# Optimization experiments

Hardware: AMD Instinct MI355X
Metric: run time of the kernel (lower is better)

The kernel has to match this reference:

```python
import jax, jax.numpy as jnp
import numpy as np

# dims
H = 1024          # hidden_size
E = 2048          # d_inner = 2*H
NH = 32           # nheads = E/64
P = 64            # headdim
N = 128           # d_state
G = 1             # ngroups
K = 4             # d_conv
Q = 128           # SSD chunk length
FF = 4096         # intermediate_size
EPS = 1e-6        # rms_norm_eps
NEPS = 1e-5       # mamba gated-norm eps
CONV_DIM = E + 2 * G * N            # 2304
D_IN = 2 * E + 2 * G * N + NH       # 4384


def rmsnorm(x, w, eps):
    v = jnp.mean(x.astype(jnp.float32) ** 2, axis=-1, keepdims=True)
    return (x.astype(jnp.float32) * jax.lax.rsqrt(v + eps)).astype(x.dtype) * w


def segsum(x):
    # x: [..., T] -> [..., T, T] with out[i,j] = sum_{j<k<=i} x[k], -inf above diag
    T = x.shape[-1]
    cs = jnp.cumsum(x, axis=-1)
    s = cs[..., :, None] - cs[..., None, :]
    mask = jnp.tril(jnp.ones((T, T), dtype=bool))
    return jnp.where(mask, s, -jnp.inf)


def ssd(x, dt, A_log, B, C):
    # x:[b,l,nh,p], dt:[b,l,nh], B,C:[b,l,N] (ngroups=1, shared over heads)
    b, l, nh, p = x.shape
    A = -jnp.exp(A_log)                      # [nh]
    dA = dt * A                              # [b,l,nh]
    xd = x * dt[..., None]                   # discretized input
    c = l // Q
    xd = xd.reshape(b, c, Q, nh, p)
    dAc = dA.reshape(b, c, Q, nh).transpose(0, 3, 1, 2)   # [b,h,c,q]
    Bc = B.reshape(b, c, Q, N)
    Cc = C.reshape(b, c, Q, N)
    A_cs = jnp.cumsum(dAc, axis=-1)                        # [b,h,c,q]
    Lm = jnp.exp(segsum(dAc))                              # [b,h,c,q,q]
    # intra-chunk (diagonal blocks)
    Y_diag = jnp.einsum('bcqn,bcsn,bhcqs,bcshp->bcqhp', Cc, Bc, Lm, xd)
    # per-chunk final states
    decay_states = jnp.exp(A_cs[..., -1:] - A_cs)          # [b,h,c,q]
    states = jnp.einsum('bcqn,bhcq,bcqhp->bchpn', Bc, decay_states, xd)
    # inter-chunk recurrence (initial state = 0)
    A_last = jnp.pad(A_cs[..., -1], ((0, 0), (0, 0), (1, 0)))   # [b,h,c+1]
    decay_chunk = jnp.exp(segsum(A_last))                       # [b,h,c+1,c+1]
    states = jnp.concatenate([jnp.zeros_like(states[:, :1]), states], axis=1)
    new_states = jnp.einsum('bhzc,bchpn->bzhpn', decay_chunk, states)[:, :-1]
    Y_off = jnp.einsum('bcqn,bchpn,bhcq->bcqhp', Cc, new_states, jnp.exp(A_cs))
    return (Y_diag + Y_off).reshape(b, l, nh, p)


def mamba2(h, w_in, w_conv, b_conv, dt_bias, A_log, D, w_mnorm, w_out):
    b, l, _ = h.shape
    zxbcdt = h @ w_in.T                         # [b,l,D_IN]
    z, xBC, dt = jnp.split(zxbcdt, [E, E + CONV_DIM], axis=-1)
    # causal depthwise conv (kernel K) over channels of xBC
    pad = jnp.pad(xBC, ((0, 0), (K - 1, 0), (0, 0)))
    xBC = sum(pad[:, k:k + l, :] * w_conv[:, k] for k in range(K)) + b_conv
    xBC = jax.nn.silu(xBC)
    x, B, C = jnp.split(xBC, [E, E + G * N], axis=-1)
    dt = jax.nn.softplus(dt + dt_bias)          # [b,l,NH]
    xh = x.reshape(b, l, NH, P)
    y = ssd(xh, dt, A_log, B, C)
    y = y + D[None, None, :, None] * xh         # per-head skip
    y = y.reshape(b, l, E)
    y = rmsnorm(y * jax.nn.silu(z), w_mnorm, NEPS)   # gated RMSNorm
    return y @ w_out.T


def setup_inputs() -> dict:
    key = jax.random.key(0)
    ks = jax.random.split(key, 12)
    dt0 = jax.random.uniform(ks[0], (NH,), minval=0.001, maxval=0.1)
    dt_bias = dt0 + jnp.log(-jnp.expm1(-dt0))   # inverse softplus
    return {
        'hidden_states': jax.random.normal(ks[1], (2, 2048, H), dtype=jnp.float32),
        'w_ln1': jnp.ones((H,), jnp.float32),
        'w_in': 0.02 * jax.random.normal(ks[2], (D_IN, H), dtype=jnp.float32),
        'w_conv': 0.1 * jax.random.normal(ks[3], (CONV_DIM, K), dtype=jnp.float32),
        'b_conv': jnp.zeros((CONV_DIM,), jnp.float32),
        'dt_bias': dt_bias,
        'A_log': jnp.log(jax.random.uniform(ks[4], (NH,), minval=1.0, maxval=16.0)),
        'D': jnp.ones((NH,), jnp.float32),
        'w_mnorm': jnp.ones((E,), jnp.float32),
        'w_out': 0.02 * jax.random.normal(ks[5], (H, E), dtype=jnp.float32),
        'w_ln2': jnp.ones((H,), jnp.float32),
        'w_gate': 0.02 * jax.random.normal(ks[6], (FF, H), dtype=jnp.float32),
        'w_up': 0.02 * jax.random.normal(ks[7], (FF, H), dtype=jnp.float32),
        'w_down': 0.02 * jax.random.normal(ks[8], (H, FF), dtype=jnp.float32),
    }


def reference(hidden_states, w_ln1, w_in, w_conv, b_conv, dt_bias, A_log, D,
              w_mnorm, w_out, w_ln2, w_gate, w_up, w_down):
    residual = hidden_states
    h = rmsnorm(hidden_states, w_ln1, EPS)
    h = mamba2(h, w_in, w_conv, b_conv, dt_bias, A_log, D, w_mnorm, w_out)
    hidden = residual + h
    residual = hidden
    h = rmsnorm(hidden, w_ln2, EPS)
    h = (jax.nn.silu(h @ w_gate.T) * (h @ w_up.T)) @ w_down.T
    return residual + h
```

## Files before the change

### kernel.cpp

```cpp
#include <hip/hip_runtime.h>

#define DEV static __device__ __forceinline__

typedef short bf16x8 __attribute__((ext_vector_type(8)));
typedef float floatx4 __attribute__((ext_vector_type(4)));
typedef unsigned short ushort4v __attribute__((ext_vector_type(4)));
typedef unsigned short ushort8v __attribute__((ext_vector_type(8)));

DEV unsigned short f32_bf16(float f) {
  unsigned int u = __builtin_bit_cast(unsigned int, f);
  u = u + 0x7fffu + ((u >> 16) & 1u);
  return (unsigned short)(u >> 16);
}
DEV float bf2f(unsigned short u) {
  unsigned int v = ((unsigned int)u) << 16;
  return __builtin_bit_cast(float, v);
}
DEV float sigmoidf_(float x) { return 1.0f / (1.0f + __expf(-x)); }
DEV float siluf_(float x) { return x * sigmoidf_(x); }

#define GLD_LDS16(g, l)                                                              \
  __builtin_amdgcn_global_load_lds((const __attribute__((address_space(1))) void*)(g), \
                                   (__attribute__((address_space(3))) void*)(l), 16, 0, 0)

template <int MODE>
__global__ __launch_bounds__(256) void gemm128(
    const unsigned short* __restrict__ A, const unsigned short* __restrict__ B,
    void* __restrict__ Cv, int K, int lda, int ldb, int ldc,
    long long bsA, long long bsB, long long bsC,
    int nsplit, unsigned short* __restrict__ Cv2, int ldc2) {
  __shared__ unsigned short As[8192];
  __shared__ unsigned short Bs[8192];
  A += (long long)blockIdx.z * bsA;
  B += (long long)blockIdx.z * bsB;
  const long long coff = (long long)blockIdx.z * bsC;
  const int tid = threadIdx.x;
  const int w = tid >> 6, lane = tid & 63;

  const int nbx = gridDim.x, nby = gridDim.y;
  const int GM = 4;
  int bid = blockIdx.y * nbx + blockIdx.x;
  int gid = bid / (GM * nbx);
  int rem = bid - gid * (GM * nbx);
  int gsz = min(GM, nby - gid * GM);
  int mtile = gid * GM + rem % gsz;
  int ntile = rem / gsz;
  const int m0 = mtile << 7, n0 = ntile << 7;

  const int srow = lane >> 2;
  const int schunk = ((lane & 3) ^ (srow & 3)) * 8;
  const unsigned short* ag0 = A + (long long)(m0 + w * 32 + srow) * lda + schunk;
  const unsigned short* ag1 = ag0 + (long long)16 * lda;
  const unsigned short* bg0 = B + (long long)(n0 + w * 32 + srow) * ldb + schunk;
  const unsigned short* bg1 = bg0 + (long long)16 * ldb;
  unsigned short* al0 = As + (w * 32) * 32 + lane * 8;
  unsigned short* al1 = As + (w * 32 + 16) * 32 + lane * 8;
  unsigned short* bl0 = Bs + (w * 32) * 32 + lane * 8;
  unsigned short* bl1 = Bs + (w * 32 + 16) * 32 + lane * 8;

  const int wr = (w >> 1) << 6, wc = (w & 1) << 6;
  const int fr = lane & 15;
  const int slot = (((lane >> 4) ^ (fr & 3))) << 3;

  floatx4 acc[4][4];
#pragma unroll
  for (int i = 0; i < 4; ++i)
#pragma unroll
    for (int j = 0; j < 4; ++j) acc[i][j] = (floatx4){0.f, 0.f, 0.f, 0.f};

  for (int k0 = 0; k0 < K; k0 += 64) {
    __syncthreads();
    GLD_LDS16(ag0 + k0, al0);
    GLD_LDS16(ag1 + k0, al1);
    GLD_LDS16(ag0 + k0 + 32, al0 + 4096);
    GLD_LDS16(ag1 + k0 + 32, al1 + 4096);
    GLD_LDS16(bg0 + k0, bl0);
    GLD_LDS16(bg1 + k0, bl1);
    GLD_LDS16(bg0 + k0 + 32, bl0 + 4096);
    GLD_LDS16(bg1 + k0 + 32, bl1 + 4096);
    __syncthreads();
#pragma unroll
    for (int s = 0; s < 2; ++s) {
      const unsigned short* Ab = As + s * 4096;
      const unsigned short* Bb = Bs + s * 4096;
      bf16x8 af[4], bf_[4];
#pragma unroll
      for (int i = 0; i < 4; ++i) af[i] = *(const bf16x8*)(Ab + (wr + i * 16 + fr) * 32 + slot);
#pragma unroll
      for (int j = 0; j < 4; ++j) bf_[j] = *(const bf16x8*)(Bb + (wc + j * 16 + fr) * 32 + slot);
#pragma unroll
      for (int i = 0; i < 4; ++i)
#pragma unroll
        for (int j = 0; j < 4; ++j)
          acc[i][j] = __builtin_amdgcn_mfma_f32_16x16x32_bf16(af[i], bf_[j], acc[i][j], 0, 0, 0);
    }
  }

  const int r0 = (lane >> 4) << 2;
#pragma unroll
  for (int i = 0; i < 4; ++i) {
#pragma unroll
    for (int j = 0; j < 4; ++j) {
      int col = n0 + wc + j * 16 + fr;
      int row = m0 + wr + i * 16 + r0;
#pragma unroll
      for (int r = 0; r < 4; ++r) {
        float v = acc[i][j][r];
        if constexpr (MODE == 0) {
          ((float*)Cv)[coff + (long long)(row + r) * ldc + col] = v;
        } else {
          if (col < nsplit)
            ((unsigned short*)Cv)[coff + (long long)(row + r) * ldc + col] = f32_bf16(v);
          else
            Cv2[(long long)(row + r) * ldc2 + (col - nsplit)] = f32_bf16(v);
        }
      }
    }
  }
}

__global__ __launch_bounds__(256) void gemm128_glu(
    const unsigned short* __restrict__ A, const unsigned short* __restrict__ Bg,
    const unsigned short* __restrict__ Bu, unsigned short* __restrict__ act,
    int K, int lda, int ldb, int ldc) {
  __shared__ unsigned short As[8192];
  __shared__ unsigned short Bgs[8192];
  __shared__ unsigned short Bus[8192];
  const int tid = threadIdx.x;
  const int w = tid >> 6, lane = tid & 63;

  const int nbx = gridDim.x, nby = gridDim.y;
  const int GM = 4;
  int bid = blockIdx.y * nbx + blockIdx.x;
  int gid = bid / (GM * nbx);
  int rem = bid - gid * (GM * nbx);
  int gsz = min(GM, nby - gid * GM);
  int mtile = gid * GM + rem % gsz;
  int ntile = rem / gsz;
  const int m0 = mtile << 7, n0 = ntile << 7;

  const int srow = lane >> 2;
  const int schunk = ((lane & 3) ^ (srow & 3)) * 8;
  const unsigned short* ag0 = A + (long long)(m0 + w * 32 + srow) * lda + schunk;
  const unsigned short* ag1 = ag0 + (long long)16 * lda;
  const unsigned short* gg0 = Bg + (long long)(n0 + w * 32 + srow) * ldb + schunk;
  const unsigned short* gg1 = gg0 + (long long)16 * ldb;
  const unsigned short* ug0 = Bu + (long long)(n0 + w * 32 + srow) * ldb + schunk;
  const unsigned short* ug1 = ug0 + (long long)16 * ldb;
  unsigned short* al0 = As + (w * 32) * 32 + lane * 8;
  unsigned short* al1 = As + (w * 32 + 16) * 32 + lane * 8;
  unsigned short* gl0 = Bgs + (w * 32) * 32 + lane * 8;
  unsigned short* gl1 = Bgs + (w * 32 + 16) * 32 + lane * 8;
  unsigned short* ul0 = Bus + (w * 32) * 32 + lane * 8;
  unsigned short* ul1 = Bus + (w * 32 + 16) * 32 + lane * 8;

  const int wr = (w >> 1) << 6, wc = (w & 1) << 6;
  const int fr = lane & 15;
  const int slot = (((lane >> 4) ^ (fr & 3))) << 3;

  floatx4 accg[4][4], accu[4][4];
#pragma unroll
  for (int i = 0; i < 4; ++i)
#pragma unroll
    for (int j = 0; j < 4; ++j) {
      accg[i][j] = (floatx4){0.f, 0.f, 0.f, 0.f};
      accu[i][j] = (floatx4){0.f, 0.f, 0.f, 0.f};
    }

  for (int k0 = 0; k0 < K; k0 += 64) {
    __syncthreads();
    GLD_LDS16(ag0 + k0, al0);
    GLD_LDS16(ag1 + k0, al1);
    GLD_LDS16(ag0 + k0 + 32, al0 + 4096);
    GLD_LDS16(ag1 + k0 + 32, al1 + 4096);
    GLD_LDS16(gg0 + k0, gl0);
    GLD_LDS16(gg1 + k0, gl1);
    GLD_LDS16(gg0 + k0 + 32, gl0 + 4096);
    GLD_LDS16(gg1 + k0 + 32, gl1 + 4096);
    GLD_LDS16(ug0 + k0, ul0);
    GLD_LDS16(ug1 + k0, ul1);
    GLD_LDS16(ug0 + k0 + 32, ul0 + 4096);
    GLD_LDS16(ug1 + k0 + 32, ul1 + 4096);
    __syncthreads();
#pragma unroll
    for (int s = 0; s < 2; ++s) {
      const unsigned short* Ab = As + s * 4096;
      const unsigned short* Gb = Bgs + s * 4096;
      const unsigned short* Ub = Bus + s * 4096;
      bf16x8 af[4], bf_[4];
#pragma unroll
      for (int i = 0; i < 4; ++i) af[i] = *(const bf16x8*)(Ab + (wr + i * 16 + fr) * 32 + slot);
#pragma unroll
      for (int j = 0; j < 4; ++j) bf_[j] = *(const bf16x8*)(Gb + (wc + j * 16 + fr) * 32 + slot);
#pragma unroll
      for (int i = 0; i < 4; ++i)
#pragma unroll
        for (int j = 0; j < 4; ++j)
          accg[i][j] = __builtin_amdgcn_mfma_f32_16x16x32_bf16(af[i], bf_[j], accg[i][j], 0, 0, 0);
#pragma unroll
      for (int j = 0; j < 4; ++j) bf_[j] = *(const bf16x8*)(Ub + (wc + j * 16 + fr) * 32 + slot);
#pragma unroll
      for (int i = 0; i < 4; ++i)
#pragma unroll
        for (int j = 0; j < 4; ++j)
          accu[i][j] = __builtin_amdgcn_mfma_f32_16x16x32_bf16(af[i], bf_[j], accu[i][j], 0, 0, 0);
    }
  }

  const int r0 = (lane >> 4) << 2;
#pragma unroll
  for (int i = 0; i < 4; ++i) {
#pragma unroll
    for (int j = 0; j < 4; ++j) {
      long long base = (long long)(m0 + wr + i * 16 + r0) * ldc + (n0 + wc + j * 16 + fr);
#pragma unroll
      for (int r = 0; r < 4; ++r)
        act[base + (long long)r * ldc] = f32_bf16(siluf_(accg[i][j][r]) * accu[i][j][r]);
    }
  }
}

template <int WM>
__global__ __launch_bounds__(256) void gemm_small_nt(
    const unsigned short* __restrict__ A, const unsigned short* __restrict__ B,
    float* __restrict__ C, int M, int N, int K, int lda, int ldb, int ldc) {
  const int w = threadIdx.x >> 6;
  const int lane = threadIdx.x & 63;
  const int lm = lane & 15;
  const int ko = (lane >> 4) << 3;
  const int bn0 = blockIdx.x << 6;
  const int m_base = blockIdx.y * (WM * 64) + w * (WM * 16);

  const unsigned short* arow[WM];
#pragma unroll
  for (int i = 0; i < WM; ++i) arow[i] = A + (long long)(m_base + i * 16 + lm) * lda + ko;
  int nv = (N - bn0) >> 4;
  nv = nv > 4 ? 4 : nv;
  const unsigned short* brow[4];
#pragma unroll
  for (int j = 0; j < 4; ++j) {
    int nr = bn0 + j * 16 + lm;
    brow[j] = B + (long long)(j < nv ? nr : 0) * ldb + ko;
  }
  floatx4 acc[WM][4];
#pragma unroll
  for (int i = 0; i < WM; ++i)
#pragma unroll
    for (int j = 0; j < 4; ++j) acc[i][j] = (floatx4){0.f, 0.f, 0.f, 0.f};
  for (int k0 = 0; k0 < K; k0 += 32) {
    bf16x8 a[WM];
#pragma unroll
    for (int i = 0; i < WM; ++i) a[i] = *(const bf16x8*)(arow[i] + k0);
#pragma unroll
    for (int j = 0; j < 4; ++j) {
      if (j < nv) {
        bf16x8 b = *(const bf16x8*)(brow[j] + k0);
#pragma unroll
        for (int i = 0; i < WM; ++i)
          acc[i][j] = __builtin_amdgcn_mfma_f32_16x16x32_bf16(a[i], b, acc[i][j], 0, 0, 0);
      }
    }
  }
  const int r0 = (lane >> 4) << 2;
#pragma unroll
  for (int i = 0; i < WM; ++i)
#pragma unroll
    for (int j = 0; j < 4; ++j)
      if (j < nv) {
        int col = bn0 + j * 16 + lm;
        long long base = (long long)(m_base + i * 16 + r0) * ldc + col;
#pragma unroll
        for (int r = 0; r < 4; ++r) C[base + (long long)r * ldc] = acc[i][j][r];
      }
}

__global__ __launch_bounds__(256) void f32_to_bf16_k(const float* __restrict__ src,
                                                     unsigned short* __restrict__ dst,
                                                     long long n4) {
  long long i = (long long)blockIdx.x * 256 + threadIdx.x;
  if (i < n4) {
    float4 v = ((const float4*)src)[i];
    ushort4v o = {f32_bf16(v.x), f32_bf16(v.y), f32_bf16(v.z), f32_bf16(v.w)};
    ((ushort4v*)dst)[i] = o;
  }
}

__global__ __launch_bounds__(256) void zero_out_k(float* __restrict__ o, long long n) {
  long long i = (long long)blockIdx.x * 256 + threadIdx.x;
  if (i < n) o[i] = 0.f;
}

__global__ __launch_bounds__(256) void rmsnorm1024_bf16_k(const float* __restrict__ x,
                                                          const float* __restrict__ w,
                                                          unsigned short* __restrict__ out,
                                                          float eps) {
  long long row = blockIdx.x;
  int t = threadIdx.x;
  float4 v = ((const float4*)(x + row * 1024))[t];
  float ss = v.x * v.x + v.y * v.y + v.z * v.z + v.w * v.w;
  __shared__ float red[4];
#pragma unroll
  for (int o = 32; o > 0; o >>= 1) ss += __shfl_down(ss, o, 64);
  if ((t & 63) == 0) red[t >> 6] = ss;
  __syncthreads();
  float tot = red[0] + red[1] + red[2] + red[3];
  float sc = rsqrtf(tot * (1.0f / 1024.0f) + eps);
  float4 wv = ((const float4*)w)[t];
  ushort4v o = {f32_bf16(v.x * sc * wv.x), f32_bf16(v.y * sc * wv.y),
                f32_bf16(v.z * sc * wv.z), f32_bf16(v.w * sc * wv.w)};
  ((ushort4v*)(out + row * 1024))[t] = o;
}

__global__ __launch_bounds__(256) void add_rmsnorm_k(const float* __restrict__ hs,
                                                     const float* __restrict__ parts,
                                                     long long pstride, int np,
                                                     const float* __restrict__ w,
                                                     float* __restrict__ mh,
                                                     unsigned short* __restrict__ h2, float eps) {
  long long row = blockIdx.x;
  int t = threadIdx.x;
  float4 v = ((const float4*)(hs + row * 1024))[t];
  for (int p = 0; p < np; ++p) {
    float4 u = ((const float4*)(parts + p * pstride + row * 1024))[t];
    v.x += u.x;
    v.y += u.y;
    v.z += u.z;
    v.w += u.w;
  }
  ((float4*)(mh + row * 1024))[t] = v;
  float ss = v.x * v.x + v.y * v.y + v.z * v.z + v.w * v.w;
  __shared__ float red[4];
#pragma unroll
  for (int o = 32; o > 0; o >>= 1) ss += __shfl_down(ss, o, 64);
  if ((t & 63) == 0) red[t >> 6] = ss;
  __syncthreads();
  float tot = red[0] + red[1] + red[2] + red[3];
  float sc = rsqrtf(tot * (1.0f / 1024.0f) + eps);
  float4 wv = ((const float4*)w)[t];
  ushort4v o = {f32_bf16(v.x * sc * wv.x), f32_bf16(v.y * sc * wv.y),
                f32_bf16(v.z * sc * wv.z), f32_bf16(v.w * sc * wv.w)};
  ((ushort4v*)(h2 + row * 1024))[t] = o;
}

__global__ __launch_bounds__(256) void addn_f32_k(const float* __restrict__ a,
                                                  const float* __restrict__ parts,
                                                  long long pstride, int np,
                                                  float* __restrict__ o, long long n4) {
  long long i = (long long)blockIdx.x * 256 + threadIdx.x;
  if (i < n4) {
    float4 x = ((const float4*)a)[i];
    for (int p = 0; p < np; ++p) {
      float4 u = ((const float4*)(parts + p * pstride))[i];
      x.x += u.x;
      x.y += u.y;
      x.z += u.z;
      x.w += u.w;
    }
    ((float4*)o)[i] = x;
  }
}

__global__ __launch_bounds__(256) void gated_rmsnorm2048_k(const unsigned short* __restrict__ y,
                                                           const unsigned short* __restrict__ z,
                                                           const float* __restrict__ w,
                                                           unsigned short* __restrict__ out,
                                                           float eps) {
  long long row = blockIdx.x;
  int t = threadIdx.x;
  ushort8v yv = ((const ushort8v*)(y + row * 2048))[t];
  ushort8v zv = ((const ushort8v*)(z + row * 2048))[t];
  float g[8];
  float ss = 0.f;
#pragma unroll
  for (int j = 0; j < 8; ++j) {
    g[j] = bf2f(yv[j]) * siluf_(bf2f(zv[j]));
    ss += g[j] * g[j];
  }
  __shared__ float red[4];
#pragma unroll
  for (int o = 32; o > 0; o >>= 1) ss += __shfl_down(ss, o, 64);
  if ((t & 63) == 0) red[t >> 6] = ss;
  __syncthreads();
  float tot = red[0] + red[1] + red[2] + red[3];
  float sc = rsqrtf(tot * (1.0f / 2048.0f) + eps);
  float ww[8];
  *(float4*)&ww[0] = ((const float4*)w)[2 * t];
  *(float4*)&ww[4] = ((const float4*)w)[2 * t + 1];
  ushort8v o;
#pragma unroll
  for (int j = 0; j < 8; ++j) o[j] = f32_bf16(g[j] * sc * ww[j]);
  ((ushort8v*)(out + row * 2048))[t] = o;
}

__global__ __launch_bounds__(256) void conv_silu_k(const unsigned short* __restrict__ xraw,
                                                   const float* __restrict__ wconv,
                                                   const float* __restrict__ bconv,
                                                   unsigned short* __restrict__ xBC) {
  int m = blockIdx.x;
  int l = m & 2047;
  for (int ch = threadIdx.x; ch < 2304; ch += 256) {
    float acc = bconv[ch];
#pragma unroll
    for (int k = 0; k < 4; ++k) {
      int lk = l + k - 3;
      if (lk >= 0) acc += bf2f(xraw[(long long)(m + k - 3) * 2304 + ch]) * wconv[ch * 4 + k];
    }
    xBC[(long long)m * 2304 + ch] = f32_bf16(siluf_(acc));
  }
}

__global__ __launch_bounds__(256) void dt_softplus_k(const float* __restrict__ dtraw,
                                                     const float* __restrict__ dt_bias,
                                                     float* __restrict__ dt_s) {
  int i = blockIdx.x * 256 + threadIdx.x;
  float xv = dtraw[i] + dt_bias[i & 31];
  dt_s[i] = xv > 20.f ? xv : log1pf(expf(xv));
}

__global__ __launch_bounds__(128) void dA_cumsum_k(const float* __restrict__ dt_s,
                                                   const float* __restrict__ A_log,
                                                   float* __restrict__ dA_cs) {
  int bi = blockIdx.x;
  int c = bi & 15, h = (bi >> 4) & 31, b = bi >> 9;
  int q = threadIdx.x;
  float A = -expf(A_log[h]);
  float v = dt_s[((long long)(b * 2048 + c * 128 + q)) * 32 + h] * A;
  __shared__ float sbuf[128];
  sbuf[q] = v;
  __syncthreads();
  for (int off = 1; off < 128; off <<= 1) {
    float tv = (q >= off) ? sbuf[q - off] : 0.f;
    __syncthreads();
    sbuf[q] += tv;
    __syncthreads();
  }
  dA_cs[(long long)bi * 128 + q] = sbuf[q];
}

__global__ __launch_bounds__(256) void ssd_diag_states_k(
    const unsigned short* __restrict__ xBC, const float* __restrict__ dt_s,
    const float* __restrict__ dA_cs, const unsigned short* __restrict__ G,
    unsigned short* __restrict__ y, unsigned short* __restrict__ states) {
  __shared__ unsigned short Mz[128 * 136];
  __shared__ unsigned short xdT[64 * 136];
  __shared__ float Acs[128];
  __shared__ float wdec[128];
  const int bx = blockIdx.x;
  const int h = bx & 31, c = (bx >> 5) & 15, b = bx >> 9;
  const int t = threadIdx.x;
  const int w = t >> 6, lane = t & 63, fr = lane & 15, hi = lane >> 4;
  const long long rowbase = (long long)b * 2048 + c * 128;
  const long long abase = ((long long)((b * 32 + h) * 16 + c)) << 7;

  if (t < 128) {
    float a = dA_cs[abase + t];
    Acs[t] = a;
    wdec[t] = __expf(dA_cs[abase + 127] - a);
  }
  {
    int s = t >> 1, p0 = (t & 1) * 32;
    float dtv = dt_s[(rowbase + s) * 32 + h];
    const ushort8v* xv = (const ushort8v*)(xBC + (rowbase + s) * 2304 + h * 64 + p0);
#pragma unroll
    for (int i = 0; i < 4; ++i) {
      ushort8v vv = xv[i];
#pragma unroll
      for (int j = 0; j < 8; ++j) xdT[(p0 + i * 8 + j) * 136 + s] = f32_bf16(bf2f(vv[j]) * dtv);
    }
  }
  __syncthreads();
  {
    int q = t >> 1, s0 = (t & 1) * 64;
    float aq = Acs[q];
    const ushort8v* gv =
        (const ushort8v*)(G + (((long long)(b * 16 + c)) * 128 + q) * 128 + s0);
#pragma unroll
    for (int i = 0; i < 8; ++i) {
      ushort8v gg = gv[i];
#pragma unroll
      for (int j = 0; j < 8; ++j) {
        int s = s0 + i * 8 + j;
        float m = (s <= q) ? bf2f(gg[j]) * __expf(aq - Acs[s]) : 0.f;
        Mz[q * 136 + s] = f32_bf16(m);
      }
    }
  }
  __syncthreads();
  const int q0 = w << 5;
  {
    floatx4 acc[2][4];
#pragma unroll
    for (int i = 0; i < 2; ++i)
#pragma unroll
      for (int j = 0; j < 4; ++j) acc[i][j] = (floatx4){0.f, 0.f, 0.f, 0.f};
#pragma unroll
    for (int k0 = 0; k0 < 128; k0 += 32) {
      int kk = k0 + hi * 8;
      bf16x8 a0 = *(const bf16x8*)(Mz + (q0 + fr) * 136 + kk);
      bf16x8 a1 = *(const bf16x8*)(Mz + (q0 + 16 + fr) * 136 + kk);
      bf16x8 bf_[4];
#pragma unroll
      for (int j = 0; j < 4; ++j) bf_[j] = *(const bf16x8*)(xdT + (j * 16 + fr) * 136 + kk);
#pragma unroll
      for (int j = 0; j < 4; ++j) {
        acc[0][j] = __builtin_amdgcn_mfma_f32_16x16x32_bf16(a0, bf_[j], acc[0][j], 0, 0, 0);
        acc[1][j] = __builtin_amdgcn_mfma_f32_16x16x32_bf16(a1, bf_[j], acc[1][j], 0, 0, 0);
      }
    }
#pragma unroll
    for (int i = 0; i < 2; ++i)
#pragma unroll
      for (int r = 0; r < 4; ++r) {
        int q = q0 + i * 16 + hi * 4 + r;
        unsigned short* yrow = y + (rowbase + q) * 2048 + h * 64;
#pragma unroll
        for (int j = 0; j < 4; ++j) yrow[j * 16 + fr] = f32_bf16(acc[i][j][r]);
      }
  }
  __syncthreads();
  {
    int s = t >> 1, n0 = (t & 1) * 64;
    float wd = wdec[s];
    const ushort8v* bv = (const ushort8v*)(xBC + (rowbase + s) * 2304 + 2048 + n0);
#pragma unroll
    for (int i = 0; i < 8; ++i) {
      ushort8v bb = bv[i];
#pragma unroll
      for (int j = 0; j < 8; ++j) Mz[(n0 + i * 8 + j) * 136 + s] = f32_bf16(bf2f(bb[j]) * wd);
    }
  }
  __syncthreads();
  {
    floatx4 acc[2][4];
#pragma unroll
    for (int i = 0; i < 2; ++i)
#pragma unroll
      for (int j = 0; j < 4; ++j) acc[i][j] = (floatx4){0.f, 0.f, 0.f, 0.f};
#pragma unroll
    for (int k0 = 0; k0 < 128; k0 += 32) {
      int kk = k0 + hi * 8;
      bf16x8 a0 = *(const bf16x8*)(Mz + (q0 + fr) * 136 + kk);
      bf16x8 a1 = *(const bf16x8*)(Mz + (q0 + 16 + fr) * 136 + kk);
      bf16x8 bf_[4];
#pragma unroll
      for (int j = 0; j < 4; ++j) bf_[j] = *(const bf16x8*)(xdT + (j * 16 + fr) * 136 + kk);
#pragma unroll
      for (int j = 0; j < 4; ++j) {
        acc[0][j] = __builtin_amdgcn_mfma_f32_16x16x32_bf16(a0, bf_[j], acc[0][j], 0, 0, 0);
        acc[1][j] = __builtin_amdgcn_mfma_f32_16x16x32_bf16(a1, bf_[j], acc[1][j], 0, 0, 0);
      }
    }
    unsigned short* st = states + (long long)bx * 8192;
#pragma unroll
    for (int i = 0; i < 2; ++i)
#pragma unroll
      for (int j = 0; j < 4; ++j) {
        int p = j * 16 + fr;
        int n = q0 + i * 16 + hi * 4;
        ushort4v o;
#pragma unroll
        for (int r = 0; r < 4; ++r) o[r] = f32_bf16(acc[i][j][r]);
        *(ushort4v*)(st + p * 128 + n) = o;
      }
  }
}

__global__ __launch_bounds__(256) void ssd_scan_k(const float* __restrict__ dA_cs,
                                                  unsigned short* __restrict__ states) {
  int h = blockIdx.x & 31, b = blockIdx.x >> 5;
  int t = threadIdx.x;
  float carry[32];
#pragma unroll
  for (int i = 0; i < 32; ++i) carry[i] = 0.f;
  for (int c = 0; c < 16; ++c) {
    long long base = ((long long)((b * 16 + c) * 32 + h)) * 8192;
    float dec = __expf(dA_cs[(((long long)((b * 32 + h) * 16 + c)) << 7) + 127]);
#pragma unroll
    for (int i = 0; i < 32; ++i) {
      long long idx = base + t + i * 256;
      float local = bf2f(states[idx]);
      states[idx] = f32_bf16(carry[i]);
      carry[i] = dec * carry[i] + local;
    }
  }
}

__global__ __launch_bounds__(256) void ssd_off_k(const unsigned short* __restrict__ xBC,
                                                 const float* __restrict__ dA_cs,
                                                 const unsigned short* __restrict__ states,
                                                 const float* __restrict__ Dvec,
                                                 unsigned short* __restrict__ y) {
  __shared__ float eA[128];
  const int bx = blockIdx.x;
  const int h = bx & 31, c = (bx >> 5) & 15, b = bx >> 9;
  const int t = threadIdx.x;
  const int w = t >> 6, lane = t & 63, fr = lane & 15, hi = lane >> 4;
  const long long rowbase = (long long)b * 2048 + c * 128;
  const long long abase = ((long long)((b * 32 + h) * 16 + c)) << 7;
  if (t < 128) eA[t] = __expf(dA_cs[abase + t]);
  __syncthreads();

  const unsigned short* st = states + (long long)bx * 8192;
  const int q0 = w << 5;
  floatx4 acc[2][4];
#pragma unroll
  for (int i = 0; i < 2; ++i)
#pragma unroll
    for (int j = 0; j < 4; ++j) acc[i][j] = (floatx4){0.f, 0.f, 0.f, 0.f};

#pragma unroll
  for (int k0 = 0; k0 < 128; k0 += 32) {
    int kk = k0 + hi * 8;
    bf16x8 a0 = *(const bf16x8*)(xBC + (rowbase + q0 + fr) * 2304 + 2176 + kk);
    bf16x8 a1 = *(const bf16x8*)(xBC + (rowbase + q0 + 16 + fr) * 2304 + 2176 + kk);
    bf16x8 bf_[4];
#pragma unroll
    for (int j = 0; j < 4; ++j) bf_[j] = *(const bf16x8*)(st + (j * 16 + fr) * 128 + kk);
#pragma unroll
    for (int j = 0; j < 4; ++j) {
      acc[0][j] = __builtin_amdgcn_mfma_f32_16x16x32_bf16(a0, bf_[j], acc[0][j], 0, 0, 0);
      acc[1][j] = __builtin_amdgcn_mfma_f32_16x16x32_bf16(a1, bf_[j], acc[1][j], 0, 0, 0);
    }
  }

  float Dh = Dvec[h];
#pragma unroll
  for (int i = 0; i < 2; ++i) {
#pragma unroll
    for (int r = 0; r < 4; ++r) {
      int q = q0 + i * 16 + hi * 4 + r;
      float e = eA[q];
      const unsigned short* xrow = xBC + (rowbase + q) * 2304 + h * 64;
      unsigned short* yrow = y + (rowbase + q) * 2048 + h * 64;
#pragma unroll
      for (int j = 0; j < 4; ++j) {
        int p = j * 16 + fr;
        float v = bf2f(yrow[p]) + e * acc[i][j][r] + Dh * bf2f(xrow[p]);
        yrow[p] = f32_bf16(v);
      }
    }
  }
}

extern "C" void kernel_launch(void* const* d_in, const int* in_sizes, int n_in, void* d_out,
                              int out_size, void* d_ws, size_t ws_size, hipStream_t stream) {
  const float* hs = (const float*)d_in[0];
  const float* w_ln1 = (const float*)d_in[1];
  const float* w_in = (const float*)d_in[2];
  const float* w_conv = (const float*)d_in[3];
  const float* b_conv = (const float*)d_in[4];
  const float* dt_bias = (const float*)d_in[5];
  const float* A_log = (const float*)d_in[6];
  const float* Dvec = (const float*)d_in[7];
  const float* w_mnorm = (const float*)d_in[8];
  const float* w_out = (const float*)d_in[9];
  const float* w_ln2 = (const float*)d_in[10];
  const float* w_gate = (const float*)d_in[11];
  const float* w_up = (const float*)d_in[12];
  const float* w_down = (const float*)d_in[13];
  float* out = (float*)d_out;
  const int M = 4096;
  const int NOSPLIT = 1 << 30;

  char* ws = (char*)d_ws;
  const size_t R0 = 0;
  const size_t R1 = 33554432;
  const size_t R1b = R1 + 33554432;
  const size_t R2 = 71303168;
  const size_t R3 = 90177536;
  const size_t R4 = 107544576;
  const size_t W0 = 108068864;
  const size_t NEED = 133234688;

  if (ws_size < NEED) {
    hipLaunchKernelGGL(zero_out_k, dim3((out_size + 255) / 256), dim3(256), 0, stream, out,
                       (long long)out_size);
    return;
  }

  unsigned short* z = (unsigned short*)(ws + R0);
  unsigned short* act = (unsigned short*)(ws + R0);
  float* oproj_parts = (float*)(ws + R0);
  unsigned short* xraw = (unsigned short*)(ws + R1);
  unsigned short* states = (unsigned short*)(ws + R1);
  unsigned short* ybuf = (unsigned short*)(ws + R1 + 16777216);
  float* down_parts = (float*)(ws + R1);
  unsigned short* wbf_out = (unsigned short*)(ws + R1b);
  unsigned short* xBC = (unsigned short*)(ws + R2);
  unsigned short* ygn = (unsigned short*)(ws + R2);
  unsigned short* h2 = (unsigned short*)(ws + R2);
  unsigned short* hnorm = (unsigned short*)(ws + R3);
  unsigned short* wbf_in = (unsigned short*)(ws + R3 + 8388608);
  float* dt_s = (float*)(ws + R3);
  float* dA_cs = (float*)(ws + R3 + 524288);
  unsigned short* Gbuf = (unsigned short*)(ws + R3 + 1048576);
  float* mh = (float*)(ws + R3);
  float* dtraw = (float*)(ws + R4);
  unsigned short* wbf_gate = (unsigned short*)(ws + W0);
  unsigned short* wbf_up = (unsigned short*)(ws + W0 + 8388608);
  unsigned short* wbf_down = (unsigned short*)(ws + W0 + 16777216);

  hipLaunchKernelGGL(rmsnorm1024_bf16_k, dim3(M), dim3(256), 0, stream, hs, w_ln1, hnorm, 1e-6f);
  hipLaunchKernelGGL(f32_to_bf16_k, dim3(4384), dim3(256), 0, stream, w_in, wbf_in, 1122304LL);
  hipLaunchKernelGGL(f32_to_bf16_k, dim3(4096), dim3(256), 0, stream, w_gate, wbf_gate, 1048576LL);
  hipLaunchKernelGGL(f32_to_bf16_k, dim3(4096), dim3(256), 0, stream, w_up, wbf_up, 1048576LL);
  hipLaunchKernelGGL(f32_to_bf16_k, dim3(4096), dim3(256), 0, stream, w_down, wbf_down, 1048576LL);
  hipLaunchKernelGGL((gemm128<1>), dim3(34, 32, 1), dim3(256), 0, stream, hnorm, wbf_in, (void*)z,
                     1024, 1024, 1024, 2048, 0LL, 0LL, 0LL, 2048, xraw, 2304);
  hipLaunchKernelGGL((gemm_small_nt<4>), dim3(1, 16, 1), dim3(256), 0, stream, hnorm,
                     wbf_in + 4352 * 1024, dtraw, M, 32, 1024, 1024, 1024, 32);
  hipLaunchKernelGGL(conv_silu_k, dim3(M), dim3(256), 0, stream, xraw, w_conv, b_conv, xBC);
  hipLaunchKernelGGL(f32_to_bf16_k, dim3(2048), dim3(256), 0, stream, w_out, wbf_out, 524288LL);
  hipLaunchKernelGGL(dt_softplus_k, dim3(512), dim3(256), 0, stream, dtraw, dt_bias, dt_s);
  hipLaunchKernelGGL(dA_cumsum_k, dim3(1024), dim3(128), 0, stream, dt_s, A_log, dA_cs);
  hipLaunchKernelGGL((gemm128<1>), dim3(1, 1, 32), dim3(256), 0, stream, xBC + 2176, xBC + 2048,
                     (void*)Gbuf, 128, 2304, 2304, 128, 294912LL, 294912LL, 16384LL, NOSPLIT,
                     (unsigned short*)nullptr, 0);
  hipLaunchKernelGGL(ssd_diag_states_k, dim3(1024), dim3(256), 0, stream, xBC, dt_s, dA_cs, Gbuf,
                     ybuf, states);
  hipLaunchKernelGGL(ssd_scan_k, dim3(64), dim3(256), 0, stream, dA_cs, states);
  hipLaunchKernelGGL(ssd_off_k, dim3(1024), dim3(256), 0, stream, xBC, dA_cs, states, Dvec, ybuf);
  hipLaunchKernelGGL(gated_rmsnorm2048_k, dim3(M), dim3(256), 0, stream, ybuf, z, w_mnorm, ygn,
                     1e-5f);
  hipLaunchKernelGGL((gemm128<0>), dim3(8, 32, 4), dim3(256), 0, stream, ygn, wbf_out,
                     (void*)oproj_parts, 512, 2048, 2048, 1024, 512LL, 512LL, 4194304LL, NOSPLIT,
                     (unsigned short*)nullptr, 0);
  hipLaunchKernelGGL(add_rmsnorm_k, dim3(M), dim3(256), 0, stream, hs, oproj_parts, 4194304LL, 4,
                     w_ln2, mh, h2, 1e-6f);
  hipLaunchKernelGGL(gemm128_glu, dim3(32, 32, 1), dim3(256), 0, stream, h2, wbf_gate, wbf_up, act,
                     1024, 1024, 1024, 4096);
  hipLaunchKernelGGL((gemm128<0>), dim3(8, 32, 2), dim3(256), 0, stream, act, wbf_down,
                     (void*)down_parts, 2048, 4096, 4096, 1024, 2048LL, 2048LL, 4194304LL, NOSPLIT,
                     (unsigned short*)nullptr, 0);
  hipLaunchKernelGGL(addn_f32_k, dim3(4096), dim3(256), 0, stream, mh, down_parts, 4194304LL, 2,
                     out, 1048576LL);
}
```

Before: 625.5 us.

## Halve gemm128 K-step, split in_proj GEMM, add SiLU-mul epilogue mode

gemm128 now stages a 32-wide K slice per iteration instead of 64, which halves its shared memory but doubles the number of barriers per K loop. The combined in_proj launch with a column-split epilogue becomes two separate launches, one for z and one for xBC, removing the per-element branch. An unused MODE 2 epilogue (SiLU times another tensor) is added. The GLU kernel's tile-grouping width goes from 4 to 8. This looks like a partial revert of an earlier K-unroll, so more synchronisation per FLOP is the main risk.

```diff
diff --git a/kernel.cpp b/kernel.cpp
--- a/kernel.cpp
+++ b/kernel.cpp
@@ -26,11 +26,10 @@
 template <int MODE>
 __global__ __launch_bounds__(256) void gemm128(
     const unsigned short* __restrict__ A, const unsigned short* __restrict__ B,
-    void* __restrict__ Cv, int K, int lda, int ldb, int ldc,
-    long long bsA, long long bsB, long long bsC,
-    int nsplit, unsigned short* __restrict__ Cv2, int ldc2) {
-  __shared__ unsigned short As[8192];
-  __shared__ unsigned short Bs[8192];
+    void* __restrict__ Cv, const unsigned short* __restrict__ other,
+    int K, int lda, int ldb, int ldc, long long bsA, long long bsB, long long bsC) {
+  __shared__ unsigned short As[4096];
+  __shared__ unsigned short Bs[4096];
   A += (long long)blockIdx.z * bsA;
   B += (long long)blockIdx.z * bsB;
   const long long coff = (long long)blockIdx.z * bsC;
@@ -68,32 +67,23 @@
 #pragma unroll
     for (int j = 0; j < 4; ++j) acc[i][j] = (floatx4){0.f, 0.f, 0.f, 0.f};
 
-  for (int k0 = 0; k0 < K; k0 += 64) {
+  for (int k0 = 0; k0 < K; k0 += 32) {
     __syncthreads();
     GLD_LDS16(ag0 + k0, al0);
     GLD_LDS16(ag1 + k0, al1);
-    GLD_LDS16(ag0 + k0 + 32, al0 + 4096);
-    GLD_LDS16(ag1 + k0 + 32, al1 + 4096);
     GLD_LDS16(bg0 + k0, bl0);
     GLD_LDS16(bg1 + k0, bl1);
-    GLD_LDS16(bg0 + k0 + 32, bl0 + 4096);
-    GLD_LDS16(bg1 + k0 + 32, bl1 + 4096);
     __syncthreads();
-#pragma unroll
-    for (int s = 0; s < 2; ++s) {
-      const unsigned short* Ab = As + s * 4096;
-      const unsigned short* Bb = Bs + s * 4096;
-      bf16x8 af[4], bf_[4];
-#pragma unroll
-      for (int i = 0; i < 4; ++i) af[i] = *(const bf16x8*)(Ab + (wr + i * 16 + fr) * 32 + slot);
-#pragma unroll
-      for (int j = 0; j < 4; ++j) bf_[j] = *(const bf16x8*)(Bb + (wc + j * 16 + fr) * 32 + slot);
-#pragma unroll
-      for (int i = 0; i < 4; ++i)
-#pragma unroll
-        for (int j = 0; j < 4; ++j)
-          acc[i][j] = __builtin_amdgcn_mfma_f32_16x16x32_bf16(af[i], bf_[j], acc[i][j], 0, 0, 0);
-    }
+    bf16x8 af[4], bf_[4];
+#pragma unroll
+    for (int i = 0; i < 4; ++i) af[i] = *(const bf16x8*)(As + (wr + i * 16 + fr) * 32 + slot);
+#pragma unroll
+    for (int j = 0; j < 4; ++j) bf_[j] = *(const bf16x8*)(Bs + (wc + j * 16 + fr) * 32 + slot);
+#pragma unroll
+    for (int i = 0; i < 4; ++i)
+#pragma unroll
+      for (int j = 0; j < 4; ++j)
+        acc[i][j] = __builtin_amdgcn_mfma_f32_16x16x32_bf16(af[i], bf_[j], acc[i][j], 0, 0, 0);
   }
 
   const int r0 = (lane >> 4) << 2;
@@ -101,18 +91,17 @@
   for (int i = 0; i < 4; ++i) {
 #pragma unroll
     for (int j = 0; j < 4; ++j) {
-      int col = n0 + wc + j * 16 + fr;
-      int row = m0 + wr + i * 16 + r0;
+      long long base = (long long)(m0 + wr + i * 16 + r0) * ldc + (n0 + wc + j * 16 + fr);
 #pragma unroll
       for (int r = 0; r < 4; ++r) {
+        long long idx = coff + base + (long long)r * ldc;
         float v = acc[i][j][r];
         if constexpr (MODE == 0) {
-          ((float*)Cv)[coff + (long long)(row + r) * ldc + col] = v;
+          ((float*)Cv)[idx] = v;
+        } else if constexpr (MODE == 1) {
+          ((unsigned short*)Cv)[idx] = f32_bf16(v);
         } else {
-          if (col < nsplit)
-            ((unsigned short*)Cv)[coff + (long long)(row + r) * ldc + col] = f32_bf16(v);
-          else
-            Cv2[(long long)(row + r) * ldc2 + (col - nsplit)] = f32_bf16(v);
+          ((unsigned short*)Cv)[idx] = f32_bf16(siluf_(v) * bf2f(other[idx]));
         }
       }
     }
@@ -130,7 +119,7 @@
   const int w = tid >> 6, lane = tid & 63;
 
   const int nbx = gridDim.x, nby = gridDim.y;
-  const int GM = 4;
+  const int GM = 8;
   int bid = blockIdx.y * nbx + blockIdx.x;
   int gid = bid / (GM * nbx);
   int rem = bid - gid * (GM * nbx);
@@ -660,7 +649,6 @@
   const float* w_down = (const float*)d_in[13];
   float* out = (float*)d_out;
   const int M = 4096;
-  const int NOSPLIT = 1 << 30;
 
   char* ws = (char*)d_ws;
   const size_t R0 = 0;
@@ -705,8 +693,11 @@
   hipLaunchKernelGGL(f32_to_bf16_k, dim3(4096), dim3(256), 0, stream, w_gate, wbf_gate, 1048576LL);
   hipLaunchKernelGGL(f32_to_bf16_k, dim3(4096), dim3(256), 0, stream, w_up, wbf_up, 1048576LL);
   hipLaunchKernelGGL(f32_to_bf16_k, dim3(4096), dim3(256), 0, stream, w_down, wbf_down, 1048576LL);
-  hipLaunchKernelGGL((gemm128<1>), dim3(34, 32, 1), dim3(256), 0, stream, hnorm, wbf_in, (void*)z,
-                     1024, 1024, 1024, 2048, 0LL, 0LL, 0LL, 2048, xraw, 2304);
+  hipLaunchKernelGGL((gemm128<1>), dim3(16, 32, 1), dim3(256), 0, stream, hnorm, wbf_in, (void*)z,
+                     (const unsigned short*)nullptr, 1024, 1024, 1024, 2048, 0LL, 0LL, 0LL);
+  hipLaunchKernelGGL((gemm128<1>), dim3(18, 32, 1), dim3(256), 0, stream, hnorm,
+                     wbf_in + 2048 * 1024, (void*)xraw, (const unsigned short*)nullptr, 1024, 1024,
+                     1024, 2304, 0LL, 0LL, 0LL);
   hipLaunchKernelGGL((gemm_small_nt<4>), dim3(1, 16, 1), dim3(256), 0, stream, hnorm,
                      wbf_in + 4352 * 1024, dtraw, M, 32, 1024, 1024, 1024, 32);
   hipLaunchKernelGGL(conv_silu_k, dim3(M), dim3(256), 0, stream, xraw, w_conv, b_conv, xBC);
@@ -714,8 +705,8 @@
   hipLaunchKernelGGL(dt_softplus_k, dim3(512), dim3(256), 0, stream, dtraw, dt_bias, dt_s);
   hipLaunchKernelGGL(dA_cumsum_k, dim3(1024), dim3(128), 0, stream, dt_s, A_log, dA_cs);
   hipLaunchKernelGGL((gemm128<1>), dim3(1, 1, 32), dim3(256), 0, stream, xBC + 2176, xBC + 2048,
-                     (void*)Gbuf, 128, 2304, 2304, 128, 294912LL, 294912LL, 16384LL, NOSPLIT,
-                     (unsigned short*)nullptr, 0);
+                     (void*)Gbuf, (const unsigned short*)nullptr, 128, 2304, 2304, 128, 294912LL,
+                     294912LL, 16384LL);
   hipLaunchKernelGGL(ssd_diag_states_k, dim3(1024), dim3(256), 0, stream, xBC, dt_s, dA_cs, Gbuf,
                      ybuf, states);
   hipLaunchKernelGGL(ssd_scan_k, dim3(64), dim3(256), 0, stream, dA_cs, states);
@@ -723,15 +714,15 @@
   hipLaunchKernelGGL(gated_rmsnorm2048_k, dim3(M), dim3(256), 0, stream, ybuf, z, w_mnorm, ygn,
                      1e-5f);
   hipLaunchKernelGGL((gemm128<0>), dim3(8, 32, 4), dim3(256), 0, stream, ygn, wbf_out,
-                     (void*)oproj_parts, 512, 2048, 2048, 1024, 512LL, 512LL, 4194304LL, NOSPLIT,
-                     (unsigned short*)nullptr, 0);
+                     (void*)oproj_parts, (const unsigned short*)nullptr, 512, 2048, 2048, 1024,
+                     512LL, 512LL, 4194304LL);
   hipLaunchKernelGGL(add_rmsnorm_k, dim3(M), dim3(256), 0, stream, hs, oproj_parts, 4194304LL, 4,
                      w_ln2, mh, h2, 1e-6f);
   hipLaunchKernelGGL(gemm128_glu, dim3(32, 32, 1), dim3(256), 0, stream, h2, wbf_gate, wbf_up, act,
                      1024, 1024, 1024, 4096);
   hipLaunchKernelGGL((gemm128<0>), dim3(8, 32, 2), dim3(256), 0, stream, act, wbf_down,
-                     (void*)down_parts, 2048, 4096, 4096, 1024, 2048LL, 2048LL, 4194304LL, NOSPLIT,
-                     (unsigned short*)nullptr, 0);
+                     (void*)down_parts, (const unsigned short*)nullptr, 2048, 4096, 4096, 1024,
+                     2048LL, 2048LL, 4194304LL);
   hipLaunchKernelGGL(addn_f32_k, dim3(4096), dim3(256), 0, stream, mh, down_parts, 4194304LL, 2,
                      out, 1048576LL);
 }
```

New measurement: 659.5 us. 1.05x slower.
